# Performance work log

Hardware: AMD Instinct MI355X
Metric: run time of the kernel (lower is better)

The kernel has to match this reference:

```python
import jax, jax.numpy as jnp
import numpy as np

NEG_SLOPE = 0.2  # PyG GATConv default negative_slope
BN_EPS = 1e-5


def _segment_softmax(logits, seg, num_segments):
    # numerically stable softmax over edges grouped by destination node
    m = jax.ops.segment_max(logits, seg, num_segments=num_segments)
    e = jnp.exp(logits - m[seg])
    s = jax.ops.segment_sum(e, seg, num_segments=num_segments)
    return e / s[seg]


def _gat_conv(x, src, dst, W, a_src, a_dst, bias, heads, d_head, concat):
    N = x.shape[0]
    h = (x @ W).reshape(N, heads, d_head)                      # [N, H, D]
    alpha_src = jnp.einsum('nhd,hd->nh', h, a_src)             # [N, H]
    alpha_dst = jnp.einsum('nhd,hd->nh', h, a_dst)             # [N, H]
    logits = jax.nn.leaky_relu(alpha_src[src] + alpha_dst[dst], NEG_SLOPE)  # [E, H]
    alpha = _segment_softmax(logits, dst, N)                   # [E, H]
    msg = h[src] * alpha[:, :, None]                           # [E, H, D]
    out = jax.ops.segment_sum(msg, dst, num_segments=N)        # [N, H, D]
    out = out.reshape(N, heads * d_head) if concat else out.mean(axis=1)
    return out + bias


def setup_inputs() -> dict:
    key = jax.random.key(0)
    ks = jax.random.split(key, 12)
    N, E = 50000, 800000
    in_dim, hidden, out_dim, heads = 256, 128, 2, 4
    d1 = hidden // heads  # 32
    s = 0.05
    return {
        'x': jax.random.normal(ks[0], (N, in_dim), dtype=jnp.float32),
        'edge_index': jax.random.randint(ks[1], (2, E), 0, N, dtype=jnp.int64),
        'W1': jax.random.normal(ks[2], (in_dim, heads * d1), dtype=jnp.float32) * s,
        'att_src1': jax.random.normal(ks[3], (heads, d1), dtype=jnp.float32) * s,
        'att_dst1': jax.random.normal(ks[4], (heads, d1), dtype=jnp.float32) * s,
        'b1': jnp.zeros((heads * d1,), dtype=jnp.float32),
        'bn_gamma': jnp.ones((hidden,), dtype=jnp.float32),
        'bn_beta': jnp.zeros((hidden,), dtype=jnp.float32),
        'bn_mean': jnp.zeros((hidden,), dtype=jnp.float32),
        'bn_var': jnp.ones((hidden,), dtype=jnp.float32),
        'W2': jax.random.normal(ks[5], (hidden, out_dim), dtype=jnp.float32) * s,
        'att_src2': jax.random.normal(ks[6], (1, out_dim), dtype=jnp.float32) * s,
        'att_dst2': jax.random.normal(ks[7], (1, out_dim), dtype=jnp.float32) * s,
        'b2': jnp.zeros((out_dim,), dtype=jnp.float32),
    }


def reference(x, edge_index, W1, att_src1, att_dst1, b1,
              bn_gamma, bn_beta, bn_mean, bn_var,
              W2, att_src2, att_dst2, b2):
    N = x.shape[0]
    # PyG GATConv adds self-loops by default
    loop = jnp.arange(N, dtype=edge_index.dtype)
    src = jnp.concatenate([edge_index[0], loop])
    dst = jnp.concatenate([edge_index[1], loop])

    heads, d1 = att_src1.shape
    h = _gat_conv(x, src, dst, W1, att_src1, att_dst1, b1, heads, d1, concat=True)
    # BatchNorm1d in eval mode (running stats), then ReLU (dropout is a no-op in eval)
    h = (h - bn_mean) * jax.lax.rsqrt(bn_var + BN_EPS) * bn_gamma + bn_beta
    h = jax.nn.relu(h)
    out = _gat_conv(h, src, dst, W2, att_src2, att_dst2, b2, 1, att_src2.shape[1], concat=False)
    return out
```

## Files before the change

kernel.cpp:

```cpp
#include <hip/hip_runtime.h>
#include <hip/hip_bf16.h>

#define LRELU(x) ((x) > 0.f ? (x) : 0.2f * (x))
#define CAP 96
#define BINBITS 7
#define BINCAP 2600

typedef short bf16x8 __attribute__((ext_vector_type(8)));
typedef float f32x4 __attribute__((ext_vector_type(4)));

__device__ __forceinline__ float b2f(unsigned short u) {
  union { unsigned int i; float f; } v;
  v.i = ((unsigned int)u) << 16;
  return v.f;
}
__device__ __forceinline__ unsigned short f2b(float f) {
  unsigned int u = __float_as_uint(f);
  unsigned int r = (u + 0x7fffu + ((u >> 16) & 1u)) >> 16;
  return (unsigned short)r;
}

__global__ __launch_bounds__(256) void prep_w1t_kernel(
    const float* __restrict__ W, unsigned short* __restrict__ w1t) {
  int idx = blockIdx.x * 256 + threadIdx.x;
  int n = idx >> 8, k = idx & 255;
  w1t[idx] = f2b(W[k * 128 + n]);
}

__global__ __launch_bounds__(256) void gemm1_mfma_kernel(
    const float* __restrict__ x, const unsigned short* __restrict__ w1t,
    const float* __restrict__ atts, const float* __restrict__ attd,
    unsigned short* __restrict__ h1bf, float* __restrict__ asrc,
    float* __restrict__ adst, int N) {
  __shared__ unsigned short bsh[128 * 264];

  const int tid = threadIdx.x;
#pragma unroll
  for (int i = 0; i < 16; i++) {
    int idx = (i * 256 + tid) * 8;
    int row = idx >> 8;
    int k = idx & 255;
    *(uint4*)(bsh + row * 264 + k) = *(const uint4*)(w1t + row * 256 + k);
  }
  __syncthreads();

  const int m0 = blockIdx.x * 64 + (tid >> 6) * 16;
  if (m0 >= N) return;
  const int lane = tid & 63;
  const int row = lane & 15;
  const int quad = lane >> 4;

  f32x4 acc[8];
#pragma unroll
  for (int t = 0; t < 8; t++) acc[t] = (f32x4){0.f, 0.f, 0.f, 0.f};

  const float* ap = x + (size_t)(m0 + row) * 256 + quad * 8;
#pragma unroll
  for (int k0 = 0; k0 < 256; k0 += 32) {
    float4 av0 = *(const float4*)(ap + k0);
    float4 av1 = *(const float4*)(ap + k0 + 4);
    float af[8] = {av0.x, av0.y, av0.z, av0.w, av1.x, av1.y, av1.z, av1.w};
    bf16x8 ahi, alo;
#pragma unroll
    for (int j = 0; j < 8; j++) {
      unsigned short h = f2b(af[j]);
      ahi[j] = (short)h;
      alo[j] = (short)f2b(af[j] - b2f(h));
    }
#pragma unroll
    for (int t = 0; t < 8; t++) {
      bf16x8 b = *(const bf16x8*)(bsh + (t * 16 + row) * 264 + k0 + quad * 8);
      acc[t] = __builtin_amdgcn_mfma_f32_16x16x32_bf16(ahi, b, acc[t], 0, 0, 0);
      acc[t] = __builtin_amdgcn_mfma_f32_16x16x32_bf16(alo, b, acc[t], 0, 0, 0);
    }
  }
  unsigned short* op = h1bf + (size_t)(m0 + quad * 4) * 128 + row;
#pragma unroll
  for (int t = 0; t < 8; t++)
#pragma unroll
    for (int r = 0; r < 4; r++)
      op[(size_t)r * 128 + t * 16] = f2b(acc[t][r]);

  float asv[8], adv[8];
#pragma unroll
  for (int t = 0; t < 8; t++) {
    asv[t] = atts[t * 16 + row];
    adv[t] = attd[t * 16 + row];
  }
  float ps[4][4], pd[4][4];
#pragma unroll
  for (int h = 0; h < 4; h++)
#pragma unroll
    for (int r = 0; r < 4; r++) {
      ps[h][r] = acc[2 * h][r] * asv[2 * h] + acc[2 * h + 1][r] * asv[2 * h + 1];
      pd[h][r] = acc[2 * h][r] * adv[2 * h] + acc[2 * h + 1][r] * adv[2 * h + 1];
    }
#pragma unroll
  for (int o = 1; o < 16; o <<= 1) {
#pragma unroll
    for (int h = 0; h < 4; h++)
#pragma unroll
      for (int r = 0; r < 4; r++) {
        ps[h][r] += __shfl_xor(ps[h][r], o);
        pd[h][r] += __shfl_xor(pd[h][r], o);
      }
  }
  if (row == 0) {
#pragma unroll
    for (int r = 0; r < 4; r++) {
      int m = m0 + quad * 4 + r;
#pragma unroll
      for (int h = 0; h < 4; h++) {
        asrc[m * 4 + h] = ps[h][r];
        adst[m * 4 + h] = pd[h][r];
      }
    }
  }
}

__global__ __launch_bounds__(256) void bin_edges_kernel(
    const int* __restrict__ ei, int E, int* __restrict__ gcnt,
    unsigned int* __restrict__ binned, int nbins) {
  __shared__ int hist[512];
  __shared__ int base[512];
  const int tid = threadIdx.x;
  for (int i = tid; i < 512; i += 256) hist[i] = 0;
  __syncthreads();
  const int chunk = (E + gridDim.x - 1) / gridDim.x;
  const int e0 = blockIdx.x * chunk;
  const int e1 = min(e0 + chunk, E);
  for (int e = e0 + tid; e < e1; e += 256)
    atomicAdd(&hist[ei[(size_t)E + e] >> BINBITS], 1);
  __syncthreads();
  for (int i = tid; i < nbins; i += 256)
    if (hist[i] > 0) base[i] = atomicAdd(&gcnt[i], hist[i]);
  __syncthreads();
  for (int i = tid; i < 512; i += 256) hist[i] = 0;
  __syncthreads();
  for (int e = e0 + tid; e < e1; e += 256) {
    int s = ei[e];
    int t = ei[(size_t)E + e];
    int b = t >> BINBITS;
    int pos = base[b] + atomicAdd(&hist[b], 1);
    if (pos < BINCAP)
      binned[(size_t)b * BINCAP + pos] = ((unsigned int)t << 16) | (unsigned int)s;
  }
}

__global__ __launch_bounds__(256) void bin_to_buckets_kernel(
    const int* __restrict__ gcnt, const unsigned int* __restrict__ binned,
    int* __restrict__ cnt, unsigned short* __restrict__ buckets, int N) {
  __shared__ unsigned short lbkt[128 * CAP];
  __shared__ int lcnt[128];
  const int b = blockIdx.x;
  const int tid = threadIdx.x;
  if (tid < 128) lcnt[tid] = 0;
  __syncthreads();
  const int ne = min(gcnt[b], BINCAP);
  const unsigned int* bp = binned + (size_t)b * BINCAP;
  for (int i = tid; i < ne; i += 256) {
    unsigned int p = bp[i];
    int ln = (p >> 16) & 127;
    int pos = atomicAdd(&lcnt[ln], 1);
    if (pos < CAP) lbkt[ln * CAP + pos] = (unsigned short)(p & 0xffff);
  }
  __syncthreads();
  const int n0 = b << BINBITS;
  const int nn = min(128, N - n0);
  if (nn <= 0) return;
  if (tid < nn) cnt[n0 + tid] = lcnt[tid];
  const int total8 = (nn * CAP) >> 3;
  uint4* d4 = (uint4*)(buckets + (size_t)n0 * CAP);
  const uint4* s4 = (const uint4*)lbkt;
  for (int i = tid; i < total8; i += 256) d4[i] = s4[i];
}

__global__ __launch_bounds__(256) void agg1_kernel(
    const int* __restrict__ cnt, const unsigned short* __restrict__ buckets,
    const unsigned short* __restrict__ h1bf, const float* __restrict__ asrc,
    const float* __restrict__ adst, const float* __restrict__ b1,
    const float* __restrict__ gamma, const float* __restrict__ beta,
    const float* __restrict__ mean, const float* __restrict__ var,
    const float* __restrict__ W2, const float* __restrict__ as2,
    const float* __restrict__ ad2, float4* __restrict__ pk, int N) {
  const int wv = __builtin_amdgcn_readfirstlane(threadIdx.x >> 6);
  const int t = blockIdx.x * 4 + wv;
  if (t >= N) return;
  const int l = threadIdx.x & 63;
  const int h = l >> 4;
  const float ad = adst[t * 4 + h];

  float acc0 = 0.f, acc1 = 0.f, den = 0.f;
  const unsigned short* bkt = buckets + (size_t)t * CAP;
  const int deg = min(__builtin_amdgcn_readfirstlane(cnt[t]), CAP);
  int j = 0;
  for (; j + 4 <= deg; j += 4) {
    int s0 = __builtin_amdgcn_readfirstlane((int)bkt[j]);
    int s1 = __builtin_amdgcn_readfirstlane((int)bkt[j + 1]);
    int s2 = __builtin_amdgcn_readfirstlane((int)bkt[j + 2]);
    int s3 = __builtin_amdgcn_readfirstlane((int)bkt[j + 3]);
    unsigned int p0 = *(const unsigned int*)(h1bf + (size_t)s0 * 128 + 2 * l);
    unsigned int p1 = *(const unsigned int*)(h1bf + (size_t)s1 * 128 + 2 * l);
    unsigned int p2 = *(const unsigned int*)(h1bf + (size_t)s2 * 128 + 2 * l);
    unsigned int p3 = *(const unsigned int*)(h1bf + (size_t)s3 * 128 + 2 * l);
    float w0 = __expf(LRELU(asrc[s0 * 4 + h] + ad));
    float w1 = __expf(LRELU(asrc[s1 * 4 + h] + ad));
    float w2 = __expf(LRELU(asrc[s2 * 4 + h] + ad));
    float w3 = __expf(LRELU(asrc[s3 * 4 + h] + ad));
    acc0 += w0 * b2f((unsigned short)(p0 & 0xffff)) +
            w1 * b2f((unsigned short)(p1 & 0xffff)) +
            w2 * b2f((unsigned short)(p2 & 0xffff)) +
            w3 * b2f((unsigned short)(p3 & 0xffff));
    acc1 += w0 * b2f((unsigned short)(p0 >> 16)) +
            w1 * b2f((unsigned short)(p1 >> 16)) +
            w2 * b2f((unsigned short)(p2 >> 16)) +
            w3 * b2f((unsigned short)(p3 >> 16));
    den += w0 + w1 + w2 + w3;
  }
  for (; j < deg; j++) {
    int s0 = __builtin_amdgcn_readfirstlane((int)bkt[j]);
    unsigned int p0 = *(const unsigned int*)(h1bf + (size_t)s0 * 128 + 2 * l);
    float w0 = __expf(LRELU(asrc[s0 * 4 + h] + ad));
    acc0 += w0 * b2f((unsigned short)(p0 & 0xffff));
    acc1 += w0 * b2f((unsigned short)(p0 >> 16));
    den += w0;
  }
  {
    unsigned int p0 = *(const unsigned int*)(h1bf + (size_t)t * 128 + 2 * l);
    float w0 = __expf(LRELU(asrc[t * 4 + h] + ad));
    acc0 += w0 * b2f((unsigned short)(p0 & 0xffff));
    acc1 += w0 * b2f((unsigned short)(p0 >> 16));
    den += w0;
  }
  const int c0 = 2 * l;
  float inv = 1.f / den;
  float v0 = acc0 * inv + b1[c0];
  float v1 = acc1 * inv + b1[c0 + 1];
  v0 = (v0 - mean[c0]) * rsqrtf(var[c0] + 1e-5f) * gamma[c0] + beta[c0];
  v1 = (v1 - mean[c0 + 1]) * rsqrtf(var[c0 + 1] + 1e-5f) * gamma[c0 + 1] +
       beta[c0 + 1];
  v0 = v0 > 0.f ? v0 : 0.f;
  v1 = v1 > 0.f ? v1 : 0.f;

  float g0 = v0 * W2[c0 * 2 + 0] + v1 * W2[(c0 + 1) * 2 + 0];
  float g1 = v0 * W2[c0 * 2 + 1] + v1 * W2[(c0 + 1) * 2 + 1];
#pragma unroll
  for (int o = 32; o > 0; o >>= 1) {
    g0 += __shfl_down(g0, o);
    g1 += __shfl_down(g1, o);
  }
  if (l == 0) {
    float4 p;
    p.x = g0;
    p.y = g1;
    p.z = g0 * as2[0] + g1 * as2[1];
    p.w = g0 * ad2[0] + g1 * ad2[1];
    pk[t] = p;
  }
}

__global__ __launch_bounds__(256) void agg2_kernel(
    const int* __restrict__ cnt, const unsigned short* __restrict__ buckets,
    const float4* __restrict__ pk, const float* __restrict__ b2,
    float* __restrict__ out, int N) {
  const int t = blockIdx.x * 16 + (threadIdx.x >> 4);
  if (t >= N) return;
  const int lg = threadIdx.x & 15;
  float4 pt = pk[t];
  const float ad = pt.w;
  float a0 = 0.f, a1 = 0.f, den = 0.f;
  const unsigned short* bkt = buckets + (size_t)t * CAP;
  const int deg = min(cnt[t], CAP);
  for (int j = lg; j < deg; j += 16) {
    float4 p = pk[bkt[j]];
    float w = __expf(LRELU(p.z + ad));
    a0 += w * p.x;
    a1 += w * p.y;
    den += w;
  }
#pragma unroll
  for (int o = 8; o > 0; o >>= 1) {
    a0 += __shfl_xor(a0, o);
    a1 += __shfl_xor(a1, o);
    den += __shfl_xor(den, o);
  }
  if (lg == 0) {
    float w = __expf(LRELU(pt.z + ad));
    a0 += w * pt.x;
    a1 += w * pt.y;
    den += w;
    float2 o2;
    o2.x = a0 / den + b2[0];
    o2.y = a1 / den + b2[1];
    *(float2*)(out + (size_t)t * 2) = o2;
  }
}

extern "C" void kernel_launch(void* const* d_in, const int* in_sizes, int n_in,
                              void* d_out, int out_size, void* d_ws,
                              size_t ws_size, hipStream_t stream) {
  const float* x      = (const float*)d_in[0];
  const int*   ei     = (const int*)d_in[1];
  const float* W1     = (const float*)d_in[2];
  const float* atts1  = (const float*)d_in[3];
  const float* attd1  = (const float*)d_in[4];
  const float* b1     = (const float*)d_in[5];
  const float* gamma  = (const float*)d_in[6];
  const float* beta   = (const float*)d_in[7];
  const float* mean   = (const float*)d_in[8];
  const float* var    = (const float*)d_in[9];
  const float* W2     = (const float*)d_in[10];
  const float* atts2  = (const float*)d_in[11];
  const float* attd2  = (const float*)d_in[12];
  const float* b2     = (const float*)d_in[13];
  float* out = (float*)d_out;

  const int N = in_sizes[0] / 256;
  const int E = in_sizes[1] / 2;
  const int nbins = (N + (1 << BINBITS) - 1) >> BINBITS;

  char* ws = (char*)d_ws;
  size_t off = 0;
  unsigned short* h1bf = (unsigned short*)(ws + off); off += (size_t)N * 128 * 2;
  float* asrc1 = (float*)(ws + off); off += (size_t)N * 4 * 4;
  float* adst1 = (float*)(ws + off); off += (size_t)N * 4 * 4;
  float4* pk   = (float4*)(ws + off); off += (size_t)N * 16;
  int*   cnt   = (int*)  (ws + off); off += (size_t)N * 4;
  int*   gcnt  = (int*)  (ws + off); off += 512 * 4;
  unsigned short* w1t = (unsigned short*)(ws + off); off += 128 * 256 * 2;
  unsigned short* buckets = (unsigned short*)(ws + off);
  off += (size_t)N * CAP * 2;
  unsigned int* binned = (unsigned int*)(ws + off);
  off += (size_t)nbins * BINCAP * 4;

  hipMemsetAsync(gcnt, 0, 512 * 4, stream);
  bin_edges_kernel<<<512, 256, 0, stream>>>(ei, E, gcnt, binned, nbins);
  bin_to_buckets_kernel<<<nbins, 256, 0, stream>>>(gcnt, binned, cnt, buckets,
                                                   N);

  prep_w1t_kernel<<<128, 256, 0, stream>>>(W1, w1t);
  gemm1_mfma_kernel<<<(N + 63) / 64, 256, 0, stream>>>(
      x, w1t, atts1, attd1, h1bf, asrc1, adst1, N);
  agg1_kernel<<<(N + 3) / 4, 256, 0, stream>>>(cnt, buckets, h1bf, asrc1,
                                               adst1, b1, gamma, beta, mean,
                                               var, W2, atts2, attd2, pk, N);

  agg2_kernel<<<(N + 15) / 16, 256, 0, stream>>>(cnt, buckets, pk, b2, out, N);
}
```

Baseline: 208.1 us.

## Precompute per-edge attention weights cooperatively in LDS before aggregation

In the first-layer aggregation kernel, each wave now computes the per-edge softmax weights once. Its 16 lanes per head each handle a subset of edges and store the weights to shared memory, and the denominator is reduced with xor shuffles. Previously every lane recomputed the exp and the asrc gather for every edge. The gather loop now reads edge indices eight at a time with vector loads, reads the weights from LDS, and accumulates with fmaf on cheap bf16 unpacks. This adds an extra pass over the bucket, LDS traffic, and a 100-slot row sized for CAP 96, so reads past deg depend on the bucket padding.

```diff
diff --git a/kernel.cpp b/kernel.cpp
--- a/kernel.cpp
+++ b/kernel.cpp
@@ -18,6 +18,15 @@
   unsigned int u = __float_as_uint(f);
   unsigned int r = (u + 0x7fffu + ((u >> 16) & 1u)) >> 16;
   return (unsigned short)r;
+}
+
+__device__ __forceinline__ void acc2(float w, unsigned int p, float& a0,
+                                     float& a1) {
+  union { unsigned int u; float f; } lo, hi;
+  lo.u = p << 16;
+  hi.u = p & 0xffff0000u;
+  a0 = fmaf(w, lo.f, a0);
+  a1 = fmaf(w, hi.f, a1);
 }
 
 __global__ __launch_bounds__(256) void prep_w1t_kernel(
@@ -183,55 +192,92 @@
     const float* __restrict__ mean, const float* __restrict__ var,
     const float* __restrict__ W2, const float* __restrict__ as2,
     const float* __restrict__ ad2, float4* __restrict__ pk, int N) {
+  __shared__ float wsh[4][4][100];
   const int wv = __builtin_amdgcn_readfirstlane(threadIdx.x >> 6);
   const int t = blockIdx.x * 4 + wv;
   if (t >= N) return;
   const int l = threadIdx.x & 63;
   const int h = l >> 4;
+  const int js = l & 15;
   const float ad = adst[t * 4 + h];
 
-  float acc0 = 0.f, acc1 = 0.f, den = 0.f;
   const unsigned short* bkt = buckets + (size_t)t * CAP;
   const int deg = min(__builtin_amdgcn_readfirstlane(cnt[t]), CAP);
+
+  float* wrow = &wsh[wv][h][0];
+  float denp = 0.f;
+  const int nb = (deg + 15) >> 4;
+  for (int b = 0; b < nb; b++) {
+    const int idx = (b << 4) + js;
+    const int s = (int)bkt[idx];
+    const float av = asrc[s * 4 + h];
+    float w = __expf(LRELU(av + ad));
+    w = (idx < deg) ? w : 0.f;
+    wrow[idx] = w;
+    denp += w;
+  }
+#pragma unroll
+  for (int o = 1; o < 16; o <<= 1) denp += __shfl_xor(denp, o);
+  const float wself = __expf(LRELU(asrc[t * 4 + h] + ad));
+  const float den = denp + wself;
+
+  float acc0 = 0.f, acc1 = 0.f;
   int j = 0;
+  for (; j + 8 <= deg; j += 8) {
+    const uint4 e4 = *(const uint4*)(bkt + j);
+    const unsigned int ea = __builtin_amdgcn_readfirstlane(e4.x);
+    const unsigned int eb = __builtin_amdgcn_readfirstlane(e4.y);
+    const unsigned int ec = __builtin_amdgcn_readfirstlane(e4.z);
+    const unsigned int ed = __builtin_amdgcn_readfirstlane(e4.w);
+    const int s0 = ea & 0xffff, s1 = ea >> 16;
+    const int s2 = eb & 0xffff, s3 = eb >> 16;
+    const int s4 = ec & 0xffff, s5 = ec >> 16;
+    const int s6 = ed & 0xffff, s7 = ed >> 16;
+    const unsigned int p0 = *(const unsigned int*)(h1bf + (size_t)s0 * 128 + 2 * l);
+    const unsigned int p1 = *(const unsigned int*)(h1bf + (size_t)s1 * 128 + 2 * l);
+    const unsigned int p2 = *(const unsigned int*)(h1bf + (size_t)s2 * 128 + 2 * l);
+    const unsigned int p3 = *(const unsigned int*)(h1bf + (size_t)s3 * 128 + 2 * l);
+    const unsigned int p4 = *(const unsigned int*)(h1bf + (size_t)s4 * 128 + 2 * l);
+    const unsigned int p5 = *(const unsigned int*)(h1bf + (size_t)s5 * 128 + 2 * l);
+    const unsigned int p6 = *(const unsigned int*)(h1bf + (size_t)s6 * 128 + 2 * l);
+    const unsigned int p7 = *(const unsigned int*)(h1bf + (size_t)s7 * 128 + 2 * l);
+    const f32x4 wa = *(const f32x4*)(wrow + j);
+    const f32x4 wb = *(const f32x4*)(wrow + j + 4);
+    acc2(wa[0], p0, acc0, acc1);
+    acc2(wa[1], p1, acc0, acc1);
+    acc2(wa[2], p2, acc0, acc1);
+    acc2(wa[3], p3, acc0, acc1);
+    acc2(wb[0], p4, acc0, acc1);
+    acc2(wb[1], p5, acc0, acc1);
+    acc2(wb[2], p6, acc0, acc1);
+    acc2(wb[3], p7, acc0, acc1);
+  }
   for (; j + 4 <= deg; j += 4) {
-    int s0 = __builtin_amdgcn_readfirstlane((int)bkt[j]);
-    int s1 = __builtin_amdgcn_readfirstlane((int)bkt[j + 1]);
-    int s2 = __builtin_amdgcn_readfirstlane((int)bkt[j + 2]);
-    int s3 = __builtin_amdgcn_readfirstlane((int)bkt[j + 3]);
-    unsigned int p0 = *(const unsigned int*)(h1bf + (size_t)s0 * 128 + 2 * l);
-    unsigned int p1 = *(const unsigned int*)(h1bf + (size_t)s1 * 128 + 2 * l);
-    unsigned int p2 = *(const unsigned int*)(h1bf + (size_t)s2 * 128 + 2 * l);
-    unsigned int p3 = *(const unsigned int*)(h1bf + (size_t)s3 * 128 + 2 * l);
-    float w0 = __expf(LRELU(asrc[s0 * 4 + h] + ad));
-    float w1 = __expf(LRELU(asrc[s1 * 4 + h] + ad));
-    float w2 = __expf(LRELU(asrc[s2 * 4 + h] + ad));
-    float w3 = __expf(LRELU(asrc[s3 * 4 + h] + ad));
-    acc0 += w0 * b2f((unsigned short)(p0 & 0xffff)) +
-            w1 * b2f((unsigned short)(p1 & 0xffff)) +
-            w2 * b2f((unsigned short)(p2 & 0xffff)) +
-            w3 * b2f((unsigned short)(p3 & 0xffff));
-    acc1 += w0 * b2f((unsigned short)(p0 >> 16)) +
-            w1 * b2f((unsigned short)(p1 >> 16)) +
-            w2 * b2f((unsigned short)(p2 >> 16)) +
-            w3 * b2f((unsigned short)(p3 >> 16));
-    den += w0 + w1 + w2 + w3;
+    const uint2 e2v = *(const uint2*)(bkt + j);
+    const unsigned int ea = __builtin_amdgcn_readfirstlane(e2v.x);
+    const unsigned int eb = __builtin_amdgcn_readfirstlane(e2v.y);
+    const int s0 = ea & 0xffff, s1 = ea >> 16;
+    const int s2 = eb & 0xffff, s3 = eb >> 16;
+    const unsigned int p0 = *(const unsigned int*)(h1bf + (size_t)s0 * 128 + 2 * l);
+    const unsigned int p1 = *(const unsigned int*)(h1bf + (size_t)s1 * 128 + 2 * l);
+    const unsigned int p2 = *(const unsigned int*)(h1bf + (size_t)s2 * 128 + 2 * l);
+    const unsigned int p3 = *(const unsigned int*)(h1bf + (size_t)s3 * 128 + 2 * l);
+    const f32x4 wa = *(const f32x4*)(wrow + j);
+    acc2(wa[0], p0, acc0, acc1);
+    acc2(wa[1], p1, acc0, acc1);
+    acc2(wa[2], p2, acc0, acc1);
+    acc2(wa[3], p3, acc0, acc1);
   }
   for (; j < deg; j++) {
-    int s0 = __builtin_amdgcn_readfirstlane((int)bkt[j]);
-    unsigned int p0 = *(const unsigned int*)(h1bf + (size_t)s0 * 128 + 2 * l);
-    float w0 = __expf(LRELU(asrc[s0 * 4 + h] + ad));
-    acc0 += w0 * b2f((unsigned short)(p0 & 0xffff));
-    acc1 += w0 * b2f((unsigned short)(p0 >> 16));
-    den += w0;
+    const int s0 = __builtin_amdgcn_readfirstlane((int)bkt[j]);
+    const unsigned int p0 = *(const unsigned int*)(h1bf + (size_t)s0 * 128 + 2 * l);
+    acc2(wrow[j], p0, acc0, acc1);
   }
   {
-    unsigned int p0 = *(const unsigned int*)(h1bf + (size_t)t * 128 + 2 * l);
-    float w0 = __expf(LRELU(asrc[t * 4 + h] + ad));
-    acc0 += w0 * b2f((unsigned short)(p0 & 0xffff));
-    acc1 += w0 * b2f((unsigned short)(p0 >> 16));
-    den += w0;
-  }
+    const unsigned int p0 = *(const unsigned int*)(h1bf + (size_t)t * 128 + 2 * l);
+    acc2(wself, p0, acc0, acc1);
+  }
+
   const int c0 = 2 * l;
   float inv = 1.f / den;
   float v0 = acc0 * inv + b1[c0];
```

New measurement: 201.1 us. -3.4%, faster.
